# Performance work log

Hardware: AMD Instinct MI355X
Metric: run time of the kernel (lower is better)

The kernel has to match this reference:

```python
import jax, jax.numpy as jnp
import numpy as np

B, T, D, H = 4, 2048, 1024, 16
HD = D // H


def setup_inputs() -> dict:
    key = jax.random.key(0)
    ks = jax.random.split(key, 6)
    x = jax.random.normal(ks[0], (B, T, D), dtype=jnp.float32)
    entity_bias = jax.random.normal(ks[1], (B, T, T), dtype=jnp.float32) * 0.02
    W_qkv = jax.random.normal(ks[2], (D, 3 * D), dtype=jnp.float32) * (1.0 / np.sqrt(D))
    b_qkv = jnp.zeros((3 * D,), dtype=jnp.float32)
    W_out = jax.random.normal(ks[3], (D, D), dtype=jnp.float32) * (1.0 / np.sqrt(D))
    b_out = jnp.zeros((D,), dtype=jnp.float32)
    return {"x": x, "entity_bias": entity_bias, "W_qkv": W_qkv, "b_qkv": b_qkv,
            "W_out": W_out, "b_out": b_out}


def reference(x, entity_bias, W_qkv, b_qkv, W_out, b_out):
    b, t, d = x.shape
    hd = d // H
    scale = hd ** -0.5
    qkv = x @ W_qkv + b_qkv                      # [B,T,3D]
    q, k, v = jnp.split(qkv, 3, axis=-1)
    sh = lambda z: z.reshape(b, t, H, hd).transpose(0, 2, 1, 3)  # [B,H,T,hd]
    q, k, v = sh(q), sh(k), sh(v)
    w = jnp.einsum('bhqd,bhkd->bhqk', q, k) * scale
    w = w + entity_bias[:, None]                 # broadcast over heads
    causal = jnp.triu(jnp.ones((t, t), dtype=bool), k=1)
    w = jnp.where(causal[None, None], jnp.float32(-1e9), w)
    a = jax.nn.softmax(w, axis=-1)
    out = jnp.einsum('bhqk,bhkd->bhqd', a, v)    # [B,H,T,hd]
    out = out.transpose(0, 2, 1, 3).reshape(b, t, d)
    return out @ W_out + b_out
```

## Files before the change

### kernel.cpp

```cpp
#include <hip/hip_runtime.h>

typedef __attribute__((ext_vector_type(8))) short short8;
typedef __attribute__((ext_vector_type(4))) short short4v;
typedef __attribute__((ext_vector_type(4))) float f32x4;

#define B_  4
#define T_  2048
#define D_  1024
#define H_  16
#define HD_ 64

#define LOG2E 1.4426950408889634f
#define QSCALE 0.1803368801111243f

__device__ __forceinline__ short f2bf(float f) {
  unsigned u = __builtin_bit_cast(unsigned, f);
  u = (u + 0x7FFFu + ((u >> 16) & 1u)) >> 16;
  return (short)u;
}
__device__ __forceinline__ short f2bf_trunc(float f) {
  return (short)(__builtin_bit_cast(unsigned, f) >> 16);
}
__device__ __forceinline__ float bf2f(short s) {
  unsigned u = ((unsigned)(unsigned short)s) << 16;
  return __builtin_bit_cast(float, u);
}

__device__ __forceinline__ void g2l16(const void* g, void* l) {
  __builtin_amdgcn_global_load_lds((const __attribute__((address_space(1))) void*)g,
                                   (__attribute__((address_space(3))) void*)l, 16, 0, 0);
}

__global__ __launch_bounds__(256) void cast_x_kernel(const float* __restrict__ src,
                                                     short* __restrict__ dst) {
  int i = (blockIdx.x * 256 + threadIdx.x) * 4;
  float4 v = *(const float4*)(src + i);
  short4v o;
  o.x = f2bf(v.x); o.y = f2bf(v.y); o.z = f2bf(v.z); o.w = f2bf(v.w);
  *(short4v*)(dst + i) = o;
}

__global__ __launch_bounds__(256) void tcast_kernel(const float* __restrict__ src,
                                                    short* __restrict__ dst, int R, int C) {
  __shared__ float tile[32][33];
  int cb = blockIdx.x, rb = blockIdx.y;
  int tr = threadIdx.x >> 5, tc = threadIdx.x & 31;
#pragma unroll
  for (int p = 0; p < 4; ++p) {
    int r = p * 8 + tr;
    tile[r][tc] = src[(size_t)(rb * 32 + r) * C + cb * 32 + tc];
  }
  __syncthreads();
#pragma unroll
  for (int p = 0; p < 4; ++p) {
    int r = p * 8 + tr;
    dst[(size_t)(cb * 32 + r) * R + rb * 32 + tc] = f2bf(tile[tc][r]);
  }
}

__global__ __launch_bounds__(512) void pb_kernel(const float* __restrict__ bias,
                                                 short* __restrict__ PB) {
  int bid = blockIdx.x;
  int b = bid / 136, tidx = bid % 136;
  int qt = 0, base = 0;
  while (base + qt + 1 <= tidx) { base += qt + 1; ++qt; }
  int kt = tidx - base;
  int tid = threadIdx.x;
  int w = tid >> 6, lane = tid & 63, quad = lane >> 4, l15 = lane & 15;
  short vals[32];
#pragma unroll
  for (int tj = 0; tj < 8; ++tj)
#pragma unroll
    for (int rr = 0; rr < 4; ++rr) {
      int ql = w * 16 + quad * 4 + rr;
      int kl = tj * 16 + l15;
      float v = bias[((size_t)b * T_ + qt * 128 + ql) * T_ + kt * 128 + kl] * LOG2E;
      if (kt == qt && kl > ql) v = -1.0e9f;
      vals[tj * 4 + rr] = f2bf(v);
    }
  short* dst = PB + ((size_t)bid * 512 + tid) * 32;
#pragma unroll
  for (int j = 0; j < 4; ++j) *(short8*)(dst + j * 8) = *(const short8*)(vals + j * 8);
}

__device__ __forceinline__ void gemm_stage(const short* __restrict__ A,
                                           const short* __restrict__ Bt, int K, int mb, int nb,
                                           int kk, short* As, short* Bs, int wave, int lane) {
#pragma unroll
  for (int i = 0; i < 2; ++i) {
    int sbase = i * 256 + wave * 64;
    int s = sbase + lane;
    int r = s >> 2;
    int cg = (s & 3) ^ ((s >> 3) & 3);
    g2l16(A + (size_t)(mb * 128 + r) * K + kk * 32 + cg * 8, As + sbase * 8);
    g2l16(Bt + (size_t)(nb * 128 + r) * K + kk * 32 + cg * 8, Bs + sbase * 8);
  }
}

__device__ __forceinline__ void gemm_compute(const short* As, const short* Bs, f32x4 acc[4][4],
                                             int quad, int l15, int wr, int wc) {
  short8 af[4], bq[4];
  int sw = quad ^ ((l15 >> 1) & 3);
#pragma unroll
  for (int t = 0; t < 4; ++t) {
    af[t] = *(const short8*)(As + ((wr * 64 + t * 16 + l15) * 4 + sw) * 8);
    bq[t] = *(const short8*)(Bs + ((wc * 64 + t * 16 + l15) * 4 + sw) * 8);
  }
#pragma unroll
  for (int i = 0; i < 4; ++i)
#pragma unroll
    for (int j = 0; j < 4; ++j)
      acc[i][j] = __builtin_amdgcn_mfma_f32_16x16x32_bf16(af[i], bq[j], acc[i][j], 0, 0, 0);
}

__device__ __forceinline__ void gemm_core(const short* __restrict__ A, const short* __restrict__ Bt,
                                          int K, int mb, int nb, short* As, short* Bs,
                                          f32x4 acc[4][4]) {
  const int tid = threadIdx.x;
  const int wave = tid >> 6, lane = tid & 63;
  const int quad = lane >> 4, l15 = lane & 15;
  const int wr = wave >> 1, wc = wave & 1;
  f32x4 zero = {0.f, 0.f, 0.f, 0.f};
#pragma unroll
  for (int i = 0; i < 4; ++i)
#pragma unroll
    for (int j = 0; j < 4; ++j) acc[i][j] = zero;

  const int nK = K >> 5;
  gemm_stage(A, Bt, K, mb, nb, 0, As, Bs, wave, lane);
  __syncthreads();
  for (int kk = 0; kk < nK - 1; ++kk) {
    int cur = kk & 1;
    gemm_stage(A, Bt, K, mb, nb, kk + 1, As + (cur ^ 1) * 4096, Bs + (cur ^ 1) * 4096, wave, lane);
    gemm_compute(As + cur * 4096, Bs + cur * 4096, acc, quad, l15, wr, wc);
    __syncthreads();
  }
  gemm_compute(As + ((nK - 1) & 1) * 4096, Bs + ((nK - 1) & 1) * 4096, acc, quad, l15, wr, wc);
}

__global__ __launch_bounds__(256, 4) void gemm_qkv_kernel(
    const short* __restrict__ xb, const short* __restrict__ Wqt, const float* __restrict__ bqkv,
    short* __restrict__ Qb, short* __restrict__ Kb, short* __restrict__ Vt) {
  __shared__ alignas(16) short As[2 * 4096];
  __shared__ alignas(16) short Bs[2 * 4096];
  f32x4 acc[4][4];
  int nb = blockIdx.x, mb = blockIdx.y;
  gemm_core(xb, Wqt, D_, mb, nb, As, Bs, acc);

  const int tid = threadIdx.x, wave = tid >> 6, lane = tid & 63;
  const int quad = lane >> 4, l15 = lane & 15;
  const int wr = wave >> 1, wc = wave & 1;
  int part = nb >> 3;
  int h = ((nb & 7) << 1) + wc;
  if (part == 2) {
#pragma unroll
    for (int j = 0; j < 4; ++j) {
      int n = nb * 128 + wc * 64 + j * 16 + l15;
      int hd = j * 16 + l15;
      float bv = bqkv[n];
#pragma unroll
      for (int i = 0; i < 4; ++i) {
        int m0 = mb * 128 + wr * 64 + i * 16 + quad * 4;
        int b = m0 >> 11, t0 = m0 & 2047;
        short4v pv;
#pragma unroll
        for (int rr = 0; rr < 4; ++rr) pv[rr] = f2bf(acc[i][j][rr] + bv);
        *(short4v*)(Vt + ((size_t)((b * H_ + h) * HD_ + hd)) * T_ + t0) = pv;
      }
    }
  } else {
    short* dst = (part == 0) ? Qb : Kb;
    float sc = (part == 0) ? QSCALE : 1.0f;
#pragma unroll
    for (int j = 0; j < 4; ++j) {
      int n = nb * 128 + wc * 64 + j * 16 + l15;
      int hd = j * 16 + l15;
      float bv = bqkv[n];
#pragma unroll
      for (int i = 0; i < 4; ++i) {
        int mrow = mb * 128 + wr * 64 + i * 16 + quad * 4;
#pragma unroll
        for (int rr = 0; rr < 4; ++rr) {
          int m = mrow + rr;
          int b = m >> 11, t = m & 2047;
          dst[((size_t)((b * H_ + h) * T_ + t)) * HD_ + hd] = f2bf((acc[i][j][rr] + bv) * sc);
        }
      }
    }
  }
}

__global__ __launch_bounds__(256, 4) void gemm_out_kernel(
    const short* __restrict__ Ob, const short* __restrict__ Wot,
    const float* __restrict__ bout, float* __restrict__ out) {
  __shared__ alignas(16) short As[2 * 4096];
  __shared__ alignas(16) short Bs[2 * 4096];
  f32x4 acc[4][4];
  int nb = blockIdx.x, mb = blockIdx.y;
  gemm_core(Ob, Wot, D_, mb, nb, As, Bs, acc);

  const int tid = threadIdx.x, wave = tid >> 6, lane = tid & 63;
  const int quad = lane >> 4, l15 = lane & 15;
  const int wr = wave >> 1, wc = wave & 1;
#pragma unroll
  for (int j = 0; j < 4; ++j) {
    int n = nb * 128 + wc * 64 + j * 16 + l15;
    float bv = bout[n];
#pragma unroll
    for (int i = 0; i < 4; ++i) {
      int mrow = mb * 128 + wr * 64 + i * 16 + quad * 4;
#pragma unroll
      for (int rr = 0; rr < 4; ++rr) {
        out[(size_t)(mrow + rr) * D_ + n] = acc[i][j][rr] + bv;
      }
    }
  }
}

__global__ __launch_bounds__(512, 2) void attn_kernel(
    const short* __restrict__ Qb, const short* __restrict__ Kb, const short* __restrict__ Vt,
    const short* __restrict__ PB, short* __restrict__ Ob) {
  __shared__ alignas(16) short Ks[2][8192];
  __shared__ alignas(16) short Vs[2][8192];
  __shared__ alignas(16) short Ps[8][512];

  const int tid = threadIdx.x, wave = tid >> 6, lane = tid & 63;
  const int quad = lane >> 4, l15 = lane & 15;
  const int bh = blockIdx.x;
  const int pair = blockIdx.y;
  const int qa = pair, qb = 15 - pair;
  const int b = bh >> 4, h = bh & 15;

  short8 aqA[2], aqB[2];
#pragma unroll
  for (int i = 0; i < 2; ++i) {
    int sbase = i * 512 + wave * 64;
    int s = sbase + lane;
    int r = s >> 3;
    int cg = (s & 7) ^ (r & 7);
    g2l16(Qb + ((size_t)bh * T_ + qa * 128 + r) * HD_ + cg * 8, &Ks[0][0] + sbase * 8);
    g2l16(Qb + ((size_t)bh * T_ + qb * 128 + r) * HD_ + cg * 8, &Vs[0][0] + sbase * 8);
  }
  __syncthreads();
  {
    int qrow = wave * 16 + l15;
#pragma unroll
    for (int c2 = 0; c2 < 2; ++c2) {
      int ch = (c2 * 4 + quad) ^ (l15 & 7);
      aqA[c2] = *(const short8*)(&Ks[0][0] + (qrow * 8 + ch) * 8);
      aqB[c2] = *(const short8*)(&Vs[0][0] + (qrow * 8 + ch) * 8);
    }
  }
  __syncthreads();

  f32x4 zero = {0.f, 0.f, 0.f, 0.f};
  f32x4 oA[4], oB[4];
  float liA[4], liB[4];
#pragma unroll
  for (int hj = 0; hj < 4; ++hj) { oA[hj] = zero; oB[hj] = zero; }
#pragma unroll
  for (int rr = 0; rr < 4; ++rr) { liA[rr] = 0.f; liB[rr] = 0.f; }

  const short* pbA = PB + ((size_t)(b * 136 + ((qa * (qa + 1)) >> 1)) * 512 + tid) * 32;
  const short* pbB = PB + ((size_t)(b * 136 + ((qb * (qb + 1)) >> 1)) * 512 + tid) * 32;
  short* pw = &Ps[wave][0];

  auto stage_kv = [&](int kt, int bufc) {
#pragma unroll
    for (int i = 0; i < 2; ++i) {
      int sbase = i * 512 + wave * 64;
      int s = sbase + lane;
      int rk = s >> 3, ck = (s & 7) ^ ((s >> 3) & 7);
      g2l16(Kb + ((size_t)bh * T_ + kt * 128 + rk) * HD_ + ck * 8, &Ks[bufc][0] + sbase * 8);
      int rv = s >> 4, cv = (s & 15) ^ ((s >> 4) & 7);
      g2l16(Vt + ((size_t)bh * HD_ + rv) * T_ + kt * 128 + cv * 8, &Vs[bufc][0] + sbase * 8);
    }
  };

  auto attn_step = [&](int kt, int bufc) {
    const short* Ksc = &Ks[bufc][0];
    const short* Vsc = &Vs[bufc][0];
    const int ks0 = quad ^ (l15 & 7), ks1 = ks0 ^ 4;
    const int vsw = l15 & 7;
#pragma unroll
    for (int tile = 0; tile < 2; ++tile) {
      if (tile == 1 && kt > qa) break;
      const short* pp = (tile == 0 ? pbB : pbA) + (size_t)kt * (512 * 32);
      const short8* aq = (tile == 0) ? aqB : aqA;
      f32x4* o = (tile == 0) ? oB : oA;
      float* li = (tile == 0) ? liB : liA;

#pragma unroll 1
      for (int half = 0; half < 2; ++half) {
        f32x4 sc[4];
#pragma unroll
        for (int j4 = 0; j4 < 2; ++j4) {
          short8 pb = *(const short8*)(pp + (half * 2 + j4) * 8);
#pragma unroll
          for (int tp = 0; tp < 2; ++tp)
#pragma unroll
            for (int rr = 0; rr < 4; ++rr) sc[j4 * 2 + tp][rr] = bf2f(pb[tp * 4 + rr]);
        }
#pragma unroll
        for (int tj = 0; tj < 4; ++tj) {
          int key = (half * 4 + tj) * 16 + l15;
          short8 bk0 = *(const short8*)(Ksc + (key * 8 + ks0) * 8);
          short8 bk1 = *(const short8*)(Ksc + (key * 8 + ks1) * 8);
          sc[tj] = __builtin_amdgcn_mfma_f32_16x16x32_bf16(aq[0], bk0, sc[tj], 0, 0, 0);
          sc[tj] = __builtin_amdgcn_mfma_f32_16x16x32_bf16(aq[1], bk1, sc[tj], 0, 0, 0);
        }

#pragma unroll
        for (int tj = 0; tj < 4; ++tj)
#pragma unroll
          for (int rr = 0; rr < 4; ++rr) {
            float p = __builtin_amdgcn_exp2f(sc[tj][rr]);
            sc[tj][rr] = p;
            li[rr] += p;
          }

#pragma unroll
        for (int kc = 0; kc < 2; ++kc) {
          int kcc = half * 2 + kc;
#pragma unroll
          for (int tp = 0; tp < 2; ++tp) {
            int tj = kc * 2 + tp;
            int klc = tp * 16 + l15;
            int hi = (klc >> 3) * 16;
#pragma unroll
            for (int rr = 0; rr < 4; ++rr) {
              pw[(hi + quad * 4 + rr) * 8 + (klc & 7)] = f2bf_trunc(sc[tj][rr]);
            }
          }
          short8 ap = *(const short8*)(pw + (quad * 16 + l15) * 8);
#pragma unroll
          for (int hj = 0; hj < 4; ++hj) {
            int hd = hj * 16 + l15;
            int tc = (kcc * 4 + quad) ^ vsw;
            short8 bv = *(const short8*)(Vsc + (hd * 16 + tc) * 8);
            o[hj] = __builtin_amdgcn_mfma_f32_16x16x32_bf16(ap, bv, o[hj], 0, 0, 0);
          }
        }
      }
    }
  };

  stage_kv(0, 0);
  __syncthreads();
  for (int kt = 0; kt < qb; ++kt) {
    int cur = kt & 1;
    stage_kv(kt + 1, cur ^ 1);
    attn_step(kt, cur);
    __syncthreads();
  }
  attn_step(qb, qb & 1);

#pragma unroll
  for (int d = 1; d < 16; d <<= 1)
#pragma unroll
    for (int rr = 0; rr < 4; ++rr) {
      liA[rr] += __shfl_xor(liA[rr], d, 64);
      liB[rr] += __shfl_xor(liB[rr], d, 64);
    }

#pragma unroll
  for (int hj = 0; hj < 4; ++hj)
#pragma unroll
    for (int rr = 0; rr < 4; ++rr) {
      int qrow = wave * 16 + quad * 4 + rr;
      int dcol = h * 64 + hj * 16 + l15;
      Ob[((size_t)b * T_ + qa * 128 + qrow) * D_ + dcol] = f2bf(oA[hj][rr] / liA[rr]);
      Ob[((size_t)b * T_ + qb * 128 + qrow) * D_ + dcol] = f2bf(oB[hj][rr] / liB[rr]);
    }
}

extern "C" void kernel_launch(void* const* d_in, const int* in_sizes, int n_in,
                              void* d_out, int out_size, void* d_ws, size_t ws_size,
                              hipStream_t stream) {
  const float* x    = (const float*)d_in[0];
  const float* bias = (const float*)d_in[1];
  const float* Wqkv = (const float*)d_in[2];
  const float* bqkv = (const float*)d_in[3];
  const float* Wout = (const float*)d_in[4];
  const float* bout = (const float*)d_in[5];
  float* out = (float*)d_out;
  char* ws = (char*)d_ws;

  short* xb   = (short*)(ws + 0);
  short* Ob   = (short*)(ws + 0);
  short* Wqt  = (short*)(ws + 16777216);
  short* Wot  = (short*)(ws + 23068672);
  short* Qb   = (short*)(ws + 25165824);
  short* Kb   = (short*)(ws + 41943040);
  short* Vt   = (short*)(ws + 58720256);
  short* PB   = (short*)(ws + 75497472);

  cast_x_kernel<<<8192, 256, 0, stream>>>(x, xb);
  tcast_kernel<<<dim3(96, 32), 256, 0, stream>>>(Wqkv, Wqt, 1024, 3072);
  tcast_kernel<<<dim3(32, 32), 256, 0, stream>>>(Wout, Wot, 1024, 1024);
  pb_kernel<<<544, 512, 0, stream>>>(bias, PB);
  gemm_qkv_kernel<<<dim3(24, 64), 256, 0, stream>>>(xb, Wqt, bqkv, Qb, Kb, Vt);
  attn_kernel<<<dim3(64, 8), 512, 0, stream>>>(Qb, Kb, Vt, PB, Ob);
  gemm_out_kernel<<<dim3(8, 64), 256, 0, stream>>>(Ob, Wot, bout, out);
}
```

Baseline: 333.9 us.

## Fuse bias preprocessing into attention kernel and merge weight transpose launches

Removes the pb_kernel that pre-packed the entity bias into bf16 tiles with LOG2E scaling and causal masking. The attention kernel now reads the fp32 bias directly from global memory and applies the scale and diagonal mask inline. The two weight transpose-cast launches are also merged into one kernel. This saves an extra pass over the bias and a launch, but the attention loop now does strided fp32 global loads per element (4-byte, row stride T) instead of one contiguous short8 load, which may cost bandwidth and latency inside the hot loop.

```diff
diff --git a/kernel.cpp b/kernel.cpp
--- a/kernel.cpp
+++ b/kernel.cpp
@@ -40,10 +40,9 @@
   *(short4v*)(dst + i) = o;
 }
 
-__global__ __launch_bounds__(256) void tcast_kernel(const float* __restrict__ src,
-                                                    short* __restrict__ dst, int R, int C) {
-  __shared__ float tile[32][33];
-  int cb = blockIdx.x, rb = blockIdx.y;
+__device__ __forceinline__ void tcast_body(const float* __restrict__ src,
+                                           short* __restrict__ dst, int R, int C,
+                                           int cb, int rb, float tile[32][33]) {
   int tr = threadIdx.x >> 5, tc = threadIdx.x & 31;
 #pragma unroll
   for (int p = 0; p < 4; ++p) {
@@ -58,29 +57,14 @@
   }
 }
 
-__global__ __launch_bounds__(512) void pb_kernel(const float* __restrict__ bias,
-                                                 short* __restrict__ PB) {
-  int bid = blockIdx.x;
-  int b = bid / 136, tidx = bid % 136;
-  int qt = 0, base = 0;
-  while (base + qt + 1 <= tidx) { base += qt + 1; ++qt; }
-  int kt = tidx - base;
-  int tid = threadIdx.x;
-  int w = tid >> 6, lane = tid & 63, quad = lane >> 4, l15 = lane & 15;
-  short vals[32];
-#pragma unroll
-  for (int tj = 0; tj < 8; ++tj)
-#pragma unroll
-    for (int rr = 0; rr < 4; ++rr) {
-      int ql = w * 16 + quad * 4 + rr;
-      int kl = tj * 16 + l15;
-      float v = bias[((size_t)b * T_ + qt * 128 + ql) * T_ + kt * 128 + kl] * LOG2E;
-      if (kt == qt && kl > ql) v = -1.0e9f;
-      vals[tj * 4 + rr] = f2bf(v);
-    }
-  short* dst = PB + ((size_t)bid * 512 + tid) * 32;
-#pragma unroll
-  for (int j = 0; j < 4; ++j) *(short8*)(dst + j * 8) = *(const short8*)(vals + j * 8);
+__global__ __launch_bounds__(256) void tcast2_kernel(const float* __restrict__ Wqkv,
+                                                     const float* __restrict__ Wout,
+                                                     short* __restrict__ Wqt,
+                                                     short* __restrict__ Wot) {
+  __shared__ float tile[32][33];
+  int cb = blockIdx.x, rb = blockIdx.y;
+  if (cb < 96) tcast_body(Wqkv, Wqt, 1024, 3072, cb, rb, tile);
+  else         tcast_body(Wout, Wot, 1024, 1024, cb - 96, rb, tile);
 }
 
 __device__ __forceinline__ void gemm_stage(const short* __restrict__ A,
@@ -219,7 +203,7 @@
 
 __global__ __launch_bounds__(512, 2) void attn_kernel(
     const short* __restrict__ Qb, const short* __restrict__ Kb, const short* __restrict__ Vt,
-    const short* __restrict__ PB, short* __restrict__ Ob) {
+    const float* __restrict__ bias, short* __restrict__ Ob) {
   __shared__ alignas(16) short Ks[2][8192];
   __shared__ alignas(16) short Vs[2][8192];
   __shared__ alignas(16) short Ps[8][512];
@@ -261,8 +245,9 @@
 #pragma unroll
   for (int rr = 0; rr < 4; ++rr) { liA[rr] = 0.f; liB[rr] = 0.f; }
 
-  const short* pbA = PB + ((size_t)(b * 136 + ((qa * (qa + 1)) >> 1)) * 512 + tid) * 32;
-  const short* pbB = PB + ((size_t)(b * 136 + ((qb * (qb + 1)) >> 1)) * 512 + tid) * 32;
+  const int ql0 = wave * 16 + quad * 4;
+  const float* bbA = bias + ((size_t)b * T_ + qa * 128 + ql0) * T_ + l15;
+  const float* bbB = bias + ((size_t)b * T_ + qb * 128 + ql0) * T_ + l15;
   short* pw = &Ps[wave][0];
 
   auto stage_kv = [&](int kt, int bufc) {
@@ -285,7 +270,9 @@
 #pragma unroll
     for (int tile = 0; tile < 2; ++tile) {
       if (tile == 1 && kt > qa) break;
-      const short* pp = (tile == 0 ? pbB : pbA) + (size_t)kt * (512 * 32);
+      const int qt = (tile == 0) ? qb : qa;
+      const float* bt = ((tile == 0) ? bbB : bbA) + kt * 128;
+      const bool diag = (kt == qt);
       const short8* aq = (tile == 0) ? aqB : aqA;
       f32x4* o = (tile == 0) ? oB : oA;
       float* li = (tile == 0) ? liB : liA;
@@ -294,13 +281,20 @@
       for (int half = 0; half < 2; ++half) {
         f32x4 sc[4];
 #pragma unroll
-        for (int j4 = 0; j4 < 2; ++j4) {
-          short8 pb = *(const short8*)(pp + (half * 2 + j4) * 8);
-#pragma unroll
-          for (int tp = 0; tp < 2; ++tp)
-#pragma unroll
-            for (int rr = 0; rr < 4; ++rr) sc[j4 * 2 + tp][rr] = bf2f(pb[tp * 4 + rr]);
-        }
+        for (int j4 = 0; j4 < 2; ++j4)
+#pragma unroll
+          for (int tp = 0; tp < 2; ++tp) {
+            int tjl = j4 * 2 + tp;
+            int tjg = half * 4 + tjl;
+            int kl = tjg * 16 + l15;
+#pragma unroll
+            for (int rr = 0; rr < 4; ++rr) {
+              float v = bt[rr * T_ + tjg * 16] * LOG2E;
+              if (diag && kl > ql0 + rr) v = -1.0e9f;
+              sc[tjl][rr] = v;
+            }
+          }
+
 #pragma unroll
         for (int tj = 0; tj < 4; ++tj) {
           int key = (half * 4 + tj) * 16 + l15;
@@ -393,13 +387,10 @@
   short* Qb   = (short*)(ws + 25165824);
   short* Kb   = (short*)(ws + 41943040);
   short* Vt   = (short*)(ws + 58720256);
-  short* PB   = (short*)(ws + 75497472);
 
   cast_x_kernel<<<8192, 256, 0, stream>>>(x, xb);
-  tcast_kernel<<<dim3(96, 32), 256, 0, stream>>>(Wqkv, Wqt, 1024, 3072);
-  tcast_kernel<<<dim3(32, 32), 256, 0, stream>>>(Wout, Wot, 1024, 1024);
-  pb_kernel<<<544, 512, 0, stream>>>(bias, PB);
+  tcast2_kernel<<<dim3(128, 32), 256, 0, stream>>>(Wqkv, Wout, Wqt, Wot);
   gemm_qkv_kernel<<<dim3(24, 64), 256, 0, stream>>>(xb, Wqt, bqkv, Qb, Kb, Vt);
-  attn_kernel<<<dim3(64, 8), 512, 0, stream>>>(Qb, Kb, Vt, PB, Ob);
+  attn_kernel<<<dim3(64, 8), 512, 0, stream>>>(Qb, Kb, Vt, bias, Ob);
   gemm_out_kernel<<<dim3(8, 64), 256, 0, stream>>>(Ob, Wot, bout, out);
 }
```

Result: slower. 361.6 us (+8.3%).
